# Kernel tuning notes

Hardware: AMD Instinct MI355X
Metric: run time of the kernel (lower is better)

Reference implementation:

```python
import jax, jax.numpy as jnp
import numpy as np

N, E = 50000, 800000
D = 64          # output_dim == d_s == d_e
H = 128         # psi hidden width
PSI_IN = 2 * D + 2 * D + D  # 320


def setup_inputs() -> dict:
    key = jax.random.key(0)
    ks = jax.random.split(key, 12)
    scale = lambda fan_in: 1.0 / np.sqrt(fan_in)
    return {
        "h_d_prev": jax.random.normal(ks[0], (N, D), jnp.float32),
        "h_s": jax.random.normal(ks[1], (N, D), jnp.float32),
        "edge_feat": jax.random.normal(ks[2], (E, D), jnp.float32),
        "sender": jax.random.randint(ks[3], (E,), 0, N, jnp.int32),
        "receiver": jax.random.randint(ks[4], (E,), 0, N, jnp.int32),
        # psi MLP params (all layers use relu, incl. last: final_activation=None)
        "W0": jax.random.normal(ks[5], (PSI_IN, H), jnp.float32) * scale(PSI_IN),
        "b0": jnp.zeros((H,), jnp.float32),
        "W1": jax.random.normal(ks[6], (H, H), jnp.float32) * scale(H),
        "b1": jnp.zeros((H,), jnp.float32),
        "W2": jax.random.normal(ks[7], (H, D), jnp.float32) * scale(H),
        "b2": jnp.zeros((D,), jnp.float32),
        # final linear transform W (no bias)
        "Wm": jax.random.normal(ks[8], (D, D), jnp.float32) * scale(D),
    }


def reference(h_d_prev, h_s, edge_feat, sender, receiver, W0, b0, W1, b1, W2, b2, Wm):
    # gather node feats to edges
    h_di = h_d_prev[sender]      # [E, D]
    h_dj = h_d_prev[receiver]    # [E, D]
    h_si = h_s[sender]           # [E, D]
    h_sj = h_s[receiver]         # [E, D]
    psi_in = jnp.concatenate([h_si, h_sj, h_di, h_dj, edge_feat], axis=-1)  # [E, 320]
    # psi MLP: relu on every layer (final_activation=None keeps default relu)
    x = jax.nn.relu(psi_in @ W0 + b0)
    x = jax.nn.relu(x @ W1 + b1)
    psi = jax.nn.relu(x @ W2 + b2)          # [E, D]
    s_ij = psi * (h_dj - h_di)              # [E, D]
    agg = jax.ops.segment_sum(s_ij, receiver, num_segments=h_d_prev.shape[0])  # [N, D]
    return h_d_prev + agg @ Wm
```

## Files before the change

kernel.cpp:

```cpp
#include <hip/hip_runtime.h>

#define NN   50000
#define EE   800000
#define DD   64
#define HH   128
#define KIN  320
#define TILE_E 64

typedef __bf16 bf16x8 __attribute__((ext_vector_type(8)));
typedef float  f32x4  __attribute__((ext_vector_type(4)));

#if __has_builtin(__builtin_amdgcn_cvt_pk_bf16_f32)
typedef __bf16 bf16x2_t __attribute__((ext_vector_type(2)));
__device__ __forceinline__ unsigned int pk2(float a, float b) {
  union { bf16x2_t v; unsigned int u; } cv;
  cv.v = __builtin_amdgcn_cvt_pk_bf16_f32(a, b);
  return cv.u;
}
__device__ __forceinline__ unsigned short f2bf(float a) {
  return (unsigned short)(pk2(a, a) & 0xFFFFu);
}
#else
__device__ __forceinline__ unsigned short f2bf(float f) {
  union { float f; unsigned int u; } v; v.f = f;
  unsigned int u = v.u + 0x7FFFu + ((v.u >> 16) & 1u);
  return (unsigned short)(u >> 16);
}
__device__ __forceinline__ unsigned int pk2(float a, float b) {
  return (unsigned int)f2bf(a) | ((unsigned int)f2bf(b) << 16);
}
#endif

__device__ __forceinline__ float bf2f(unsigned short b) {
  union { unsigned int u; float f; } v; v.u = ((unsigned int)b) << 16; return v.f;
}

__device__ __forceinline__ int psiIdx(int row, int kk) {
  return ((((row >> 4) * 10 + (kk >> 5)) << 6) + ((row & 15) << 2) + ((kk >> 3) & 3)) * 8
         + (kk & 7);
}

__global__ __launch_bounds__(256) void prep_weights(
    const float* __restrict__ W0,
    const float* __restrict__ W1,
    const float* __restrict__ W2,
    unsigned short* __restrict__ WT0,
    unsigned short* __restrict__ WT1,
    unsigned short* __restrict__ WT2) {
  int t = blockIdx.x * 256 + threadIdx.x;
  if (t < KIN * HH) {
    int k = t / HH, n = t % HH;
    WT0[n * KIN + k] = f2bf(W0[t]);
  } else if (t < KIN * HH + HH * HH) {
    int u = t - KIN * HH; int k = u / HH, n = u % HH;
    WT1[n * HH + k] = f2bf(W1[u]);
  } else {
    int u = t - KIN * HH - HH * HH; int k = u / DD, n = u % DD;
    WT2[n * HH + k] = f2bf(W2[u]);
  }
}

__global__ __launch_bounds__(256, 4) void edge_mlp(
    const float* __restrict__ hd,
    const float* __restrict__ hs,
    const float* __restrict__ ef,
    const int* __restrict__ snd,
    const int* __restrict__ rcv,
    const unsigned short* __restrict__ WT0,
    const float* __restrict__ b0,
    const unsigned short* __restrict__ WT1,
    const float* __restrict__ b1,
    const unsigned short* __restrict__ WT2,
    const float* __restrict__ b2,
    float* __restrict__ agg)
{
  __shared__ __align__(16) unsigned short psi[TILE_E * KIN];

  const int tid  = threadIdx.x;
  const int e0   = blockIdx.x * TILE_E;
  const int wv   = tid >> 6;
  const int lane = tid & 63;
  const int ln   = lane & 15;
  const int quad = lane >> 4;

  int ridx[16];
  #pragma unroll
  for (int mt = 0; mt < 4; ++mt)
    #pragma unroll
    for (int i = 0; i < 4; ++i)
      ridx[mt * 4 + i] = rcv[e0 + mt * 16 + quad * 4 + i];

  #pragma unroll
  for (int i = 0; i < 10; ++i) {
    const int seg = i >> 1;
    int e = ((i << 5) + (tid >> 3)) & 63;
    int c = tid & 7;
    const float* src;
    if      (seg == 0) src = hs + (size_t)snd[e0 + e] * DD;
    else if (seg == 1) src = hs + (size_t)rcv[e0 + e] * DD;
    else if (seg == 2) src = hd + (size_t)snd[e0 + e] * DD;
    else if (seg == 3) src = hd + (size_t)rcv[e0 + e] * DD;
    else               src = ef + (size_t)(e0 + e) * DD;
    float4 v0 = *(const float4*)(src + c * 8);
    float4 v1 = *(const float4*)(src + c * 8 + 4);
    uint4 w;
    w.x = pk2(v0.x, v0.y); w.y = pk2(v0.z, v0.w);
    w.z = pk2(v1.x, v1.y); w.w = pk2(v1.z, v1.w);
    int unit = (((e >> 4) * 10 + seg * 2 + (c >> 2)) << 6) + ((e & 15) << 2) + (c & 3);
    *(uint4*)(&psi[unit * 8]) = w;
  }
  __syncthreads();

  f32x4 acc0[4], acc1[4];

  {
    #pragma unroll
    for (int m = 0; m < 4; ++m) { acc0[m] = (f32x4){0,0,0,0}; acc1[m] = (f32x4){0,0,0,0}; }
    const unsigned short* wb0 = WT0 + (wv * 32 + ln) * KIN + quad * 8;
    const unsigned short* wb1 = wb0 + 16 * KIN;
    #pragma unroll
    for (int k0 = 0; k0 < 10; ++k0) {
      bf16x8 bf0 = *(const bf16x8*)(wb0 + k0 * 32);
      bf16x8 bf1 = *(const bf16x8*)(wb1 + k0 * 32);
      #pragma unroll
      for (int mt = 0; mt < 4; ++mt) {
        bf16x8 af = *(const bf16x8*)(&psi[(((mt * 10 + k0) << 6) + (ln << 2) + quad) * 8]);
        acc0[mt] = __builtin_amdgcn_mfma_f32_16x16x32_bf16(af, bf0, acc0[mt], 0, 0, 0);
        acc1[mt] = __builtin_amdgcn_mfma_f32_16x16x32_bf16(af, bf1, acc1[mt], 0, 0, 0);
      }
    }
  }
  __syncthreads();

  {
    float bv0 = b0[wv * 32 + ln];
    float bv1 = b0[wv * 32 + 16 + ln];
    #pragma unroll
    for (int mt = 0; mt < 4; ++mt) {
      #pragma unroll
      for (int i = 0; i < 4; ++i) {
        int base = ((mt * 10 + wv) << 6) + ((quad * 4 + i) << 2) + (ln >> 3);
        float v0 = acc0[mt][i] + bv0; v0 = v0 > 0.f ? v0 : 0.f;
        float v1 = acc1[mt][i] + bv1; v1 = v1 > 0.f ? v1 : 0.f;
        psi[base * 8 + (ln & 7)]       = f2bf(v0);
        psi[(base + 2) * 8 + (ln & 7)] = f2bf(v1);
      }
    }
  }
  __syncthreads();

  {
    #pragma unroll
    for (int m = 0; m < 4; ++m) { acc0[m] = (f32x4){0,0,0,0}; acc1[m] = (f32x4){0,0,0,0}; }
    const unsigned short* wb0 = WT1 + (wv * 32 + ln) * HH + quad * 8;
    const unsigned short* wb1 = wb0 + 16 * HH;
    #pragma unroll
    for (int k0 = 0; k0 < 4; ++k0) {
      bf16x8 bf0 = *(const bf16x8*)(wb0 + k0 * 32);
      bf16x8 bf1 = *(const bf16x8*)(wb1 + k0 * 32);
      #pragma unroll
      for (int mt = 0; mt < 4; ++mt) {
        bf16x8 af = *(const bf16x8*)(&psi[(((mt * 10 + k0) << 6) + (ln << 2) + quad) * 8]);
        acc0[mt] = __builtin_amdgcn_mfma_f32_16x16x32_bf16(af, bf0, acc0[mt], 0, 0, 0);
        acc1[mt] = __builtin_amdgcn_mfma_f32_16x16x32_bf16(af, bf1, acc1[mt], 0, 0, 0);
      }
    }
  }
  __syncthreads();

  {
    float bv0 = b1[wv * 32 + ln];
    float bv1 = b1[wv * 32 + 16 + ln];
    #pragma unroll
    for (int mt = 0; mt < 4; ++mt) {
      #pragma unroll
      for (int i = 0; i < 4; ++i) {
        int base = ((mt * 10 + wv) << 6) + ((quad * 4 + i) << 2) + (ln >> 3);
        float v0 = acc0[mt][i] + bv0; v0 = v0 > 0.f ? v0 : 0.f;
        float v1 = acc1[mt][i] + bv1; v1 = v1 > 0.f ? v1 : 0.f;
        psi[base * 8 + (ln & 7)]       = f2bf(v0);
        psi[(base + 2) * 8 + (ln & 7)] = f2bf(v1);
      }
    }
  }
  __syncthreads();

  {
    f32x4 acc[4];
    #pragma unroll
    for (int m = 0; m < 4; ++m) acc[m] = (f32x4){0,0,0,0};
    const unsigned short* wb = WT2 + (wv * 16 + ln) * HH + quad * 8;
    #pragma unroll
    for (int k0 = 0; k0 < 4; ++k0) {
      bf16x8 bf = *(const bf16x8*)(wb + k0 * 32);
      #pragma unroll
      for (int mt = 0; mt < 4; ++mt) {
        bf16x8 af = *(const bf16x8*)(&psi[(((mt * 10 + k0) << 6) + (ln << 2) + quad) * 8]);
        acc[mt] = __builtin_amdgcn_mfma_f32_16x16x32_bf16(af, bf, acc[mt], 0, 0, 0);
      }
    }
    int   col = wv * 16 + ln;
    float bv  = b2[col];
    #pragma unroll
    for (int mt = 0; mt < 4; ++mt) {
      #pragma unroll
      for (int i = 0; i < 4; ++i) {
        int row = mt * 16 + quad * 4 + i;
        float p  = acc[mt][i] + bv; p = p > 0.f ? p : 0.f;
        float di = bf2f(psi[psiIdx(row, 128 + col)]);
        float dj = bf2f(psi[psiIdx(row, 192 + col)]);
        float s  = p * (dj - di);
        atomicAdd(&agg[(size_t)ridx[mt * 4 + i] * DD + col], s);
      }
    }
  }
}

__global__ __launch_bounds__(256) void final_out(
    const float* __restrict__ hd,
    const float* __restrict__ agg,
    const float* __restrict__ Wm,
    float* __restrict__ out)
{
  __shared__ float wmf[DD * DD];
  int tid = threadIdx.x;
  #pragma unroll
  for (int i = tid; i < DD * DD; i += 256) wmf[i] = Wm[i];
  __syncthreads();

  int row = blockIdx.x * 4 + (tid >> 6);
  int c   = tid & 63;
  const float* ar = agg + (size_t)row * DD;
  float s = 0.f;
  #pragma unroll
  for (int k = 0; k < DD; ++k) s += ar[k] * wmf[k * DD + c];
  size_t o = (size_t)row * DD + c;
  out[o] = hd[o] + s;
}

extern "C" void kernel_launch(void* const* d_in, const int* in_sizes, int n_in,
                              void* d_out, int out_size, void* d_ws, size_t ws_size,
                              hipStream_t stream) {
  const float* hd = (const float*)d_in[0];
  const float* hs = (const float*)d_in[1];
  const float* ef = (const float*)d_in[2];
  const int* snd  = (const int*)d_in[3];
  const int* rcv  = (const int*)d_in[4];
  const float* W0 = (const float*)d_in[5];
  const float* b0 = (const float*)d_in[6];
  const float* W1 = (const float*)d_in[7];
  const float* b1 = (const float*)d_in[8];
  const float* W2 = (const float*)d_in[9];
  const float* b2 = (const float*)d_in[10];
  const float* Wm = (const float*)d_in[11];
  float* out      = (float*)d_out;

  char* ws = (char*)d_ws;
  float* agg = (float*)ws;
  unsigned short* WT0 = (unsigned short*)(ws + 12800000);
  unsigned short* WT1 = WT0 + KIN * HH;
  unsigned short* WT2 = WT1 + HH * HH;

  hipMemsetAsync(agg, 0, (size_t)NN * DD * sizeof(float), stream);
  prep_weights<<<256, 256, 0, stream>>>(W0, W1, W2, WT0, WT1, WT2);
  edge_mlp<<<EE / TILE_E, 256, 0, stream>>>(hd, hs, ef, snd, rcv,
                                            WT0, b0, WT1, b1, WT2, b2, agg);
  final_out<<<NN / 4, 256, 0, stream>>>(hd, agg, Wm, out);
}
```

Baseline: 587.0 us.

## Pre-convert node tables to bf16 and vectorize final output projection

Adds a pre-pass that converts h_d_prev and h_s to bf16 tables, so the edge kernel's four random gathers per edge move half the bytes and skip the per-edge fp32-to-bf16 packing. The final output kernel now handles 16 rows per block, stages the agg rows in shared memory and computes four output columns per thread with vector loads and stores. The cost is an extra kernel launch plus about 12.8 MB of extra workspace traffic for the converted tables.

```diff
diff --git a/kernel.cpp b/kernel.cpp
--- a/kernel.cpp
+++ b/kernel.cpp
@@ -60,9 +60,25 @@
   }
 }
 
+__global__ __launch_bounds__(256) void prep_tables(
+    const float* __restrict__ hd, const float* __restrict__ hs,
+    unsigned short* __restrict__ hdb, unsigned short* __restrict__ hsb) {
+  int t = blockIdx.x * 256 + threadIdx.x;
+  const int n = NN * DD / 8;
+  const float* src; unsigned short* dst; int i;
+  if (t < n) { src = hd; dst = hdb; i = t; }
+  else       { src = hs; dst = hsb; i = t - n; }
+  float4 a = *(const float4*)(src + (size_t)i * 8);
+  float4 b = *(const float4*)(src + (size_t)i * 8 + 4);
+  uint4 w;
+  w.x = pk2(a.x, a.y); w.y = pk2(a.z, a.w);
+  w.z = pk2(b.x, b.y); w.w = pk2(b.z, b.w);
+  *(uint4*)(dst + (size_t)i * 8) = w;
+}
+
 __global__ __launch_bounds__(256, 4) void edge_mlp(
-    const float* __restrict__ hd,
-    const float* __restrict__ hs,
+    const unsigned short* __restrict__ hdb,
+    const unsigned short* __restrict__ hsb,
     const float* __restrict__ ef,
     const int* __restrict__ snd,
     const int* __restrict__ rcv,
@@ -95,18 +111,19 @@
     const int seg = i >> 1;
     int e = ((i << 5) + (tid >> 3)) & 63;
     int c = tid & 7;
-    const float* src;
-    if      (seg == 0) src = hs + (size_t)snd[e0 + e] * DD;
-    else if (seg == 1) src = hs + (size_t)rcv[e0 + e] * DD;
-    else if (seg == 2) src = hd + (size_t)snd[e0 + e] * DD;
-    else if (seg == 3) src = hd + (size_t)rcv[e0 + e] * DD;
-    else               src = ef + (size_t)(e0 + e) * DD;
-    float4 v0 = *(const float4*)(src + c * 8);
-    float4 v1 = *(const float4*)(src + c * 8 + 4);
+    int unit = (((e >> 4) * 10 + seg * 2 + (c >> 2)) << 6) + ((e & 15) << 2) + (c & 3);
     uint4 w;
-    w.x = pk2(v0.x, v0.y); w.y = pk2(v0.z, v0.w);
-    w.z = pk2(v1.x, v1.y); w.w = pk2(v1.z, v1.w);
-    int unit = (((e >> 4) * 10 + seg * 2 + (c >> 2)) << 6) + ((e & 15) << 2) + (c & 3);
+    if (seg < 4) {
+      const unsigned short* tb = (seg & 2) ? hdb : hsb;
+      const int* ix = (seg & 1) ? rcv : snd;
+      w = *(const uint4*)(tb + (size_t)ix[e0 + e] * DD + c * 8);
+    } else {
+      const float* src = ef + (size_t)(e0 + e) * DD;
+      float4 v0 = *(const float4*)(src + c * 8);
+      float4 v1 = *(const float4*)(src + c * 8 + 4);
+      w.x = pk2(v0.x, v0.y); w.y = pk2(v0.z, v0.w);
+      w.z = pk2(v1.x, v1.y); w.w = pk2(v1.z, v1.w);
+    }
     *(uint4*)(&psi[unit * 8]) = w;
   }
   __syncthreads();
@@ -223,19 +240,33 @@
     float* __restrict__ out)
 {
   __shared__ float wmf[DD * DD];
+  __shared__ float arow[16 * 72];
   int tid = threadIdx.x;
+  const float4* wm4 = (const float4*)Wm;
+  float4* wf4 = (float4*)wmf;
   #pragma unroll
-  for (int i = tid; i < DD * DD; i += 256) wmf[i] = Wm[i];
-  __syncthreads();
-
-  int row = blockIdx.x * 4 + (tid >> 6);
-  int c   = tid & 63;
-  const float* ar = agg + (size_t)row * DD;
-  float s = 0.f;
+  for (int i = tid; i < DD * DD / 4; i += 256) wf4[i] = wm4[i];
+
+  int r0 = blockIdx.x * 16;
+  {
+    float4 av = *(const float4*)(agg + (size_t)r0 * DD + tid * 4);
+    int rr = tid >> 4, cc = (tid & 15) * 4;
+    *(float4*)&arow[rr * 72 + cc] = av;
+  }
+  __syncthreads();
+
+  int row = tid >> 4;
+  int cq  = (tid & 15) * 4;
+  f32x4 acc = (f32x4){0, 0, 0, 0};
   #pragma unroll
-  for (int k = 0; k < DD; ++k) s += ar[k] * wmf[k * DD + c];
-  size_t o = (size_t)row * DD + c;
-  out[o] = hd[o] + s;
+  for (int k = 0; k < DD; ++k) {
+    float a = arow[row * 72 + k];
+    f32x4 w = *(const f32x4*)&wmf[k * DD + cq];
+    acc += a * w;
+  }
+  size_t o = ((size_t)(r0 + row)) * DD + cq;
+  f32x4 h = *(const f32x4*)(hd + o);
+  *(f32x4*)(out + o) = h + acc;
 }
 
 extern "C" void kernel_launch(void* const* d_in, const int* in_sizes, int n_in,
@@ -260,10 +291,12 @@
   unsigned short* WT0 = (unsigned short*)(ws + 12800000);
   unsigned short* WT1 = WT0 + KIN * HH;
   unsigned short* WT2 = WT1 + HH * HH;
-
+  unsigned short* hdb = WT2 + HH * DD;
+  unsigned short* hsb = hdb + (size_t)NN * DD;
   hipMemsetAsync(agg, 0, (size_t)NN * DD * sizeof(float), stream);
   prep_weights<<<256, 256, 0, stream>>>(W0, W1, W2, WT0, WT1, WT2);
-  edge_mlp<<<EE / TILE_E, 256, 0, stream>>>(hd, hs, ef, snd, rcv,
+  prep_tables<<<NN * DD * 2 / 8 / 256, 256, 0, stream>>>(hd, hs, hdb, hsb);
+  edge_mlp<<<EE / TILE_E, 256, 0, stream>>>(hdb, hsb, ef, snd, rcv,
                                             WT0, b0, WT1, b1, WT2, b2, agg);
-  final_out<<<NN / 4, 256, 0, stream>>>(hd, agg, Wm, out);
-}
+  final_out<<<NN / 16, 256, 0, stream>>>(hd, agg, Wm, out);
+}
```

Measured after the change: 536.8 us. 8.6% less time.
